# Kernel optimization log

Measured on AMD Instinct MI355X. Metric: run time of the kernel, lower is better.

Reference implementation:

```python
import jax, jax.numpy as jnp
import numpy as np

B = 512        # number of graphs in the batch
NP = 512       # nodes per graph (max segment length)
N = B * NP     # total nodes
D = 256        # in_feats
K = 32         # top-k nodes kept per graph


def setup_inputs() -> dict:
    key = jax.random.key(0)
    k1, k2 = jax.random.split(key, 2)
    feat = jax.random.normal(k1, (N, D), dtype=jnp.float32)
    w = jax.random.normal(k2, (1, D), dtype=jnp.float32) / np.sqrt(D)  # nn.Linear(in_feats, 1) weight
    b = jnp.zeros((1,), dtype=jnp.float32)                              # nn.Linear bias
    segment_ids = jnp.repeat(jnp.arange(B, dtype=jnp.int32), NP)        # sorted graph id per node
    return {"feat": feat, "w": w, "b": b, "segment_ids": segment_ids}


def reference(feat, w, b, segment_ids):
    # gate = self.att(feat) -> (N, 1) -> (N,)
    gate = (feat @ w.T + b)[:, 0]

    # dgl.softmax_nodes: numerically stable segment softmax per graph
    gmax = jax.ops.segment_max(gate, segment_ids, num_segments=B)
    e = jnp.exp(gate - gmax[segment_ids])
    denom = jax.ops.segment_sum(e, segment_ids, num_segments=B)
    gate_sm = e / denom[segment_ids]                                    # (N,)

    # position of each node within its segment (supports ragged segments)
    counts = jax.ops.segment_sum(jnp.ones((N,), jnp.int32), segment_ids, num_segments=B)
    offsets = jnp.concatenate([jnp.zeros((1,), jnp.int32), jnp.cumsum(counts)[:-1].astype(jnp.int32)])
    pos = jnp.arange(N, dtype=jnp.int32) - offsets[segment_ids]

    # scatter gates into dense (B, NP) padded with -inf, keep node ids alongside
    neg_inf = jnp.finfo(jnp.float32).min
    dense_gate = jnp.full((B, NP), neg_inf, jnp.float32).at[segment_ids, pos].set(gate_sm)
    dense_nid = jnp.zeros((B, NP), jnp.int32).at[segment_ids, pos].set(jnp.arange(N, dtype=jnp.int32))

    # dgl.topk_nodes: per-graph top-k by gate, gather node features -> (B, K, D)
    _, cols = jax.lax.top_k(dense_gate, K)
    node_idx = jnp.take_along_axis(dense_nid, cols, axis=1)             # (B, K) global node ids
    return feat[node_idx]                                               # (B, K, D)
```

## Files before the change

### kernel.cpp

```cpp
#include <hip/hip_runtime.h>

#define D   256
#define NP  512
#define BG  512
#define K   32
#define D4  (D/4)

__global__ __launch_bounds__(256) void gate_kernel(const float* __restrict__ feat,
                                                   const float* __restrict__ w,
                                                   const float* __restrict__ b,
                                                   float* __restrict__ gate,
                                                   int n_rows) {
    const int lane   = threadIdx.x & 63;
    const int wave   = (blockIdx.x * blockDim.x + threadIdx.x) >> 6;
    const int nwaves = (gridDim.x * blockDim.x) >> 6;

    const float4 w4  = ((const float4*)w)[lane];
    const float bias = b[0];
    const float4* f4 = (const float4*)feat;

    for (int row = wave; row < n_rows; row += nwaves) {
        float4 f = f4[(size_t)row * D4 + lane];
        float s = f.x * w4.x + f.y * w4.y + f.z * w4.z + f.w * w4.w;
        #pragma unroll
        for (int off = 32; off; off >>= 1)
            s += __shfl_xor(s, off, 64);
        if (lane == 0) gate[row] = s + bias;
    }
}

__global__ __launch_bounds__(256) void topk_kernel(const float* __restrict__ feat,
                                                   const float* __restrict__ gate,
                                                   float* __restrict__ out) {
    __shared__ float sval[NP];
    __shared__ int   sidx[NP];
    __shared__ float red[4];
    __shared__ float s_bcast;

    const int g    = blockIdx.x;
    const int tid  = threadIdx.x;
    const int lane = tid & 63;
    const int wid  = tid >> 6;

    const float v0 = gate[g * NP + tid];
    const float v1 = gate[g * NP + tid + 256];

    float m = fmaxf(v0, v1);
    #pragma unroll
    for (int off = 32; off; off >>= 1)
        m = fmaxf(m, __shfl_xor(m, off, 64));
    if (lane == 0) red[wid] = m;
    __syncthreads();
    if (tid == 0) s_bcast = fmaxf(fmaxf(red[0], red[1]), fmaxf(red[2], red[3]));
    __syncthreads();
    const float gmax = s_bcast;

    const float e0 = expf(v0 - gmax);
    const float e1 = expf(v1 - gmax);
    float s = e0 + e1;
    #pragma unroll
    for (int off = 32; off; off >>= 1)
        s += __shfl_xor(s, off, 64);
    __syncthreads();
    if (lane == 0) red[wid] = s;
    __syncthreads();
    if (tid == 0) s_bcast = (red[0] + red[1]) + (red[2] + red[3]);
    __syncthreads();
    const float denom = s_bcast;

    sval[tid]        = e0 / denom;  sidx[tid]        = tid;
    sval[tid + 256]  = e1 / denom;  sidx[tid + 256]  = tid + 256;
    __syncthreads();

    for (int k = 2; k <= NP; k <<= 1) {
        for (int j = k >> 1; j > 0; j >>= 1) {
            #pragma unroll
            for (int rep = 0; rep < 2; ++rep) {
                int t = tid + rep * 256;
                int ixj = t ^ j;
                if (ixj > t) {
                    float va = sval[t],  vb = sval[ixj];
                    int   ia = sidx[t],  ib = sidx[ixj];
                    bool b_first = (vb > va) || (vb == va && ib < ia);
                    bool do_swap = ((t & k) == 0) ? b_first : !b_first;
                    if (do_swap) {
                        sval[t] = vb; sval[ixj] = va;
                        sidx[t] = ib; sidx[ixj] = ia;
                    }
                }
            }
            __syncthreads();
        }
    }

    const float4* f4 = (const float4*)feat;
    float4*       o4 = (float4*)out;
    #pragma unroll
    for (int q = tid; q < K * D4; q += 256) {
        int r = q >> 6;
        int c = q & 63;
        int node = g * NP + sidx[r];
        o4[((size_t)(g * K + r)) * D4 + c] = f4[(size_t)node * D4 + c];
    }
}

extern "C" void kernel_launch(void* const* d_in, const int* in_sizes, int n_in,
                              void* d_out, int out_size, void* d_ws, size_t ws_size,
                              hipStream_t stream) {
    const float* feat = (const float*)d_in[0];
    const float* w    = (const float*)d_in[1];
    const float* b    = (const float*)d_in[2];

    const int n_rows = in_sizes[0] / D;
    float* gate = (float*)d_ws;
    float* out  = (float*)d_out;

    gate_kernel<<<2048, 256, 0, stream>>>(feat, w, b, gate, n_rows);
    topk_kernel<<<BG, 256, 0, stream>>>(feat, gate, out);
}
```

Before: 379.6 us.

## Fuse gate GEMV into per-graph top-k kernel with packed 64-bit sort keys

Merges the gate dot-product kernel into the per-graph softmax/top-k kernel, so each block computes gates for its own 512 rows directly into shared memory, with four rows in flight per wave. This removes the intermediate gate buffer round-trip and one kernel launch. The bitonic sort now works on packed 64-bit keys (probability bits in the high word, reversed index in the low word), which halves shared-memory traffic per compare-swap and removes the tie-break branch. The trade-off is that only 512 blocks stream the 256MB feature matrix, down from 2048 in the old gate kernel, which may reduce memory-level parallelism.

```diff
diff --git a/kernel.cpp b/kernel.cpp
--- a/kernel.cpp
+++ b/kernel.cpp
@@ -6,34 +6,12 @@
 #define K   32
 #define D4  (D/4)
 
-__global__ __launch_bounds__(256) void gate_kernel(const float* __restrict__ feat,
-                                                   const float* __restrict__ w,
-                                                   const float* __restrict__ b,
-                                                   float* __restrict__ gate,
-                                                   int n_rows) {
-    const int lane   = threadIdx.x & 63;
-    const int wave   = (blockIdx.x * blockDim.x + threadIdx.x) >> 6;
-    const int nwaves = (gridDim.x * blockDim.x) >> 6;
-
-    const float4 w4  = ((const float4*)w)[lane];
-    const float bias = b[0];
-    const float4* f4 = (const float4*)feat;
-
-    for (int row = wave; row < n_rows; row += nwaves) {
-        float4 f = f4[(size_t)row * D4 + lane];
-        float s = f.x * w4.x + f.y * w4.y + f.z * w4.z + f.w * w4.w;
-        #pragma unroll
-        for (int off = 32; off; off >>= 1)
-            s += __shfl_xor(s, off, 64);
-        if (lane == 0) gate[row] = s + bias;
-    }
-}
-
-__global__ __launch_bounds__(256) void topk_kernel(const float* __restrict__ feat,
-                                                   const float* __restrict__ gate,
-                                                   float* __restrict__ out) {
+__global__ __launch_bounds__(256) void fused_pool_kernel(const float* __restrict__ feat,
+                                                         const float* __restrict__ w,
+                                                         const float* __restrict__ b,
+                                                         float* __restrict__ out) {
     __shared__ float sval[NP];
-    __shared__ int   sidx[NP];
+    __shared__ unsigned long long skey[NP];
     __shared__ float red[4];
     __shared__ float s_bcast;
 
@@ -42,8 +20,39 @@
     const int lane = tid & 63;
     const int wid  = tid >> 6;
 
-    const float v0 = gate[g * NP + tid];
-    const float v1 = gate[g * NP + tid + 256];
+    const float4  w4   = ((const float4*)w)[lane];
+    const float   bias = b[0];
+    const float4* f4   = (const float4*)feat + (size_t)g * NP * D4;
+
+    const int rbase = wid * 128;
+    for (int i = 0; i < 128; i += 4) {
+        const int r = rbase + i;
+        float4 a0 = f4[(size_t)(r + 0) * D4 + lane];
+        float4 a1 = f4[(size_t)(r + 1) * D4 + lane];
+        float4 a2 = f4[(size_t)(r + 2) * D4 + lane];
+        float4 a3 = f4[(size_t)(r + 3) * D4 + lane];
+        float s0 = a0.x * w4.x + a0.y * w4.y + a0.z * w4.z + a0.w * w4.w;
+        float s1 = a1.x * w4.x + a1.y * w4.y + a1.z * w4.z + a1.w * w4.w;
+        float s2 = a2.x * w4.x + a2.y * w4.y + a2.z * w4.z + a2.w * w4.w;
+        float s3 = a3.x * w4.x + a3.y * w4.y + a3.z * w4.z + a3.w * w4.w;
+        #pragma unroll
+        for (int off = 32; off; off >>= 1) {
+            s0 += __shfl_xor(s0, off, 64);
+            s1 += __shfl_xor(s1, off, 64);
+            s2 += __shfl_xor(s2, off, 64);
+            s3 += __shfl_xor(s3, off, 64);
+        }
+        if (lane == 0) {
+            sval[r + 0] = s0 + bias;
+            sval[r + 1] = s1 + bias;
+            sval[r + 2] = s2 + bias;
+            sval[r + 3] = s3 + bias;
+        }
+    }
+    __syncthreads();
+
+    const float v0 = sval[tid];
+    const float v1 = sval[tid + 256];
 
     float m = fmaxf(v0, v1);
     #pragma unroll
@@ -68,8 +77,12 @@
     __syncthreads();
     const float denom = s_bcast;
 
-    sval[tid]        = e0 / denom;  sidx[tid]        = tid;
-    sval[tid + 256]  = e1 / denom;  sidx[tid + 256]  = tid + 256;
+    const float p0 = e0 / denom;
+    const float p1 = e1 / denom;
+    skey[tid] = ((unsigned long long)__float_as_uint(p0) << 32)
+              | (unsigned)(NP - 1 - tid);
+    skey[tid + 256] = ((unsigned long long)__float_as_uint(p1) << 32)
+                    | (unsigned)(NP - 1 - (tid + 256));
     __syncthreads();
 
     for (int k = 2; k <= NP; k <<= 1) {
@@ -79,28 +92,23 @@
                 int t = tid + rep * 256;
                 int ixj = t ^ j;
                 if (ixj > t) {
-                    float va = sval[t],  vb = sval[ixj];
-                    int   ia = sidx[t],  ib = sidx[ixj];
-                    bool b_first = (vb > va) || (vb == va && ib < ia);
+                    unsigned long long ka = skey[t], kb = skey[ixj];
+                    bool b_first = kb > ka;
                     bool do_swap = ((t & k) == 0) ? b_first : !b_first;
-                    if (do_swap) {
-                        sval[t] = vb; sval[ixj] = va;
-                        sidx[t] = ib; sidx[ixj] = ia;
-                    }
+                    if (do_swap) { skey[t] = kb; skey[ixj] = ka; }
                 }
             }
             __syncthreads();
         }
     }
 
-    const float4* f4 = (const float4*)feat;
-    float4*       o4 = (float4*)out;
+    float4* o4 = (float4*)out + (size_t)g * K * D4;
     #pragma unroll
     for (int q = tid; q < K * D4; q += 256) {
         int r = q >> 6;
         int c = q & 63;
-        int node = g * NP + sidx[r];
-        o4[((size_t)(g * K + r)) * D4 + c] = f4[(size_t)node * D4 + c];
+        int row = NP - 1 - (int)(unsigned)(skey[r] & 0xffffffffULL);
+        o4[q] = f4[(size_t)row * D4 + c];
     }
 }
 
@@ -111,10 +119,5 @@
     const float* w    = (const float*)d_in[1];
     const float* b    = (const float*)d_in[2];
 
-    const int n_rows = in_sizes[0] / D;
-    float* gate = (float*)d_ws;
-    float* out  = (float*)d_out;
-
-    gate_kernel<<<2048, 256, 0, stream>>>(feat, w, b, gate, n_rows);
-    topk_kernel<<<BG, 256, 0, stream>>>(feat, gate, out);
+    fused_pool_kernel<<<BG, 256, 0, stream>>>(feat, w, b, (float*)d_out);
 }
```

New measurement: 379.9 us. No clear change (+0.1%).
